# Optimization experiments

Hardware: AMD Instinct MI355X
Metric: run time of the kernel (lower is better)

## Reference

```python
import jax, jax.numpy as jnp
import numpy as np

NPHEN = 64    # number of expert submodels
K = 32        # len(subset1): selected experts / output columns
B = 2048      # batch size
D_IN = 1024   # input feature dim
HID = 2048    # hidden dim of each expert MLP


def setup_inputs() -> dict:
    key = jax.random.key(0)
    k_x, k_s, k_w1, k_b1, k_w2, k_b2 = jax.random.split(key, 6)
    x = jax.random.normal(k_x, (B, D_IN), dtype=jnp.float32)
    subset1 = jax.random.randint(k_s, (K,), 0, NPHEN, dtype=jnp.int64)
    # Expert parameter banks (one 2-layer MLP per phenotype), scaled like torch defaults
    W1 = jax.random.normal(k_w1, (NPHEN, D_IN, HID), dtype=jnp.float32) / np.sqrt(D_IN)
    b1 = jax.random.normal(k_b1, (NPHEN, HID), dtype=jnp.float32) * 0.01
    W2 = jax.random.normal(k_w2, (NPHEN, HID, 1), dtype=jnp.float32) / np.sqrt(HID)
    b2 = jax.random.normal(k_b2, (NPHEN, 1), dtype=jnp.float32) * 0.01
    return {"x": x, "subset1": subset1, "W1": W1, "b1": b1, "W2": W2, "b2": b2}


def reference(x, subset1, W1, b1, W2, b2):
    # Gather the selected experts' weights: [K, D_IN, HID], [K, HID], [K, HID], [K]
    W1s = W1[subset1]
    b1s = b1[subset1]
    W2s = W2[subset1, :, 0]
    b2s = b2[subset1, 0]
    # Batched grouped matmul replacing the per-column Python loop:
    # h[b,k,h] = relu(sum_d x[b,d] * W1s[k,d,h] + b1s[k,h])
    h = jax.nn.relu(jnp.einsum('bd,kdh->bkh', x, W1s) + b1s[None, :, :])
    # predVector[b,k] = sum_h h[b,k,h] * W2s[k,h] + b2s[k]  (== modelList[subset1[k]](x)[:,0])
    pred = jnp.einsum('bkh,kh->bk', h, W2s) + b2s[None, :]
    return pred
```

## Files before the change

kernel.cpp:

```cpp
#include <hip/hip_runtime.h>

#define D_IN 1024
#define HID  2048
#define KSEL 32

typedef __attribute__((ext_vector_type(8))) short short8;
typedef __attribute__((ext_vector_type(4))) float f32x4;

__device__ __forceinline__ short f2bf(float f) {
  union { float f; unsigned u; } c; c.f = f;
  unsigned u = c.u;
  unsigned r = (u + 0x7fffu + ((u >> 16) & 1u)) >> 16;
  return (short)(r & 0xffffu);
}

__global__ __launch_bounds__(256) void conv_x_kernel(const float* __restrict__ x,
                                                     short* __restrict__ Apanel) {
  int tid = blockIdx.x * 256 + threadIdx.x;
  int k8 = tid & 3;
  int m  = (tid >> 2) & 127;
  int ks = (tid >> 9) & 31;
  int mt = tid >> 14;
  const float* src = x + (size_t)(mt * 128 + m) * D_IN + ks * 32 + k8 * 8;
  short8 v;
#pragma unroll
  for (int j = 0; j < 8; ++j) v[j] = f2bf(src[j]);
  *(short8*)(Apanel + (size_t)tid * 8) = v;
}

__global__ __launch_bounds__(256) void conv_w1_kernel(const float* __restrict__ W1,
                                                      const int* __restrict__ subset,
                                                      short* __restrict__ Bpanel) {
  int bid = blockIdx.x;
  int ks = bid & 31;
  int nt = (bid >> 5) & 15;
  int kk = bid >> 9;
  int p  = subset[kk];
  __shared__ float tile[32][129];
  int t = threadIdx.x;
  const float* src = W1 + ((size_t)p * D_IN + ks * 32) * HID + nt * 128;
#pragma unroll
  for (int i = 0; i < 4; ++i) {
    int dl = i * 8 + (t >> 5);
    int hl = (t & 31) * 4;
    float4 v = *(const float4*)(src + (size_t)dl * HID + hl);
    tile[dl][hl] = v.x; tile[dl][hl + 1] = v.y;
    tile[dl][hl + 2] = v.z; tile[dl][hl + 3] = v.w;
  }
  __syncthreads();
  short* dst = Bpanel + (size_t)((kk * 16 + nt) * 32 + ks) * 4096;
#pragma unroll
  for (int j = 0; j < 2; ++j) {
    int n  = j * 64 + (t >> 2);
    int d8 = (t & 3) * 8;
    short8 v;
#pragma unroll
    for (int dd = 0; dd < 8; ++dd) v[dd] = f2bf(tile[d8 + dd][n]);
    *(short8*)(dst + n * 32 + d8) = v;
  }
}

__global__ __launch_bounds__(256) void init_out_kernel(const int* __restrict__ subset,
                                                       const float* __restrict__ b2,
                                                       float* __restrict__ out) {
  int i = blockIdx.x * 256 + threadIdx.x;
  out[i] = b2[subset[i & 31]];
}

__device__ __forceinline__ void load_lds16(const short* g, short* l) {
  __builtin_amdgcn_global_load_lds((const __attribute__((address_space(1))) void*)g,
                                   (__attribute__((address_space(3))) void*)l,
                                   16, 0, 0);
}

__global__ __launch_bounds__(256) void gemm_kernel(const short* __restrict__ Apanel,
                                                   const short* __restrict__ Bpanel,
                                                   const int* __restrict__ subset,
                                                   const float* __restrict__ b1,
                                                   const float* __restrict__ W2,
                                                   float* __restrict__ out) {
  __shared__ __align__(16) short Atile[4096];
  __shared__ __align__(16) short Btile[4096];

  int id = blockIdx.x;
  int xcd = id & 7;
  int chunk = id >> 3;
  int kk = xcd * 4 + (chunk >> 8);
  int nt = (chunk >> 4) & 15;
  int mt = chunk & 15;

  int tid  = threadIdx.x;
  int wave = tid >> 6;
  int lane = tid & 63;
  int wm = wave >> 1, wn = wave & 1;
  int ml = lane & 15;
  int kq = lane >> 4;

  const short* Abase = Apanel + (size_t)mt * (32 * 4096);
  const short* Bbase = Bpanel + (size_t)((kk * 16 + nt)) * (32 * 4096);

  short* AldsBase0 = Atile + (wave * 64) * 8;
  short* AldsBase1 = Atile + (256 + wave * 64) * 8;
  short* BldsBase0 = Btile + (wave * 64) * 8;
  short* BldsBase1 = Btile + (256 + wave * 64) * 8;

  f32x4 acc[4][4] = {};

  const short8* Ar = (const short8*)Atile;
  const short8* Br = (const short8*)Btile;
  int arow = wm * 64 + ml;
  int brow = wn * 64 + ml;

  for (int ks = 0; ks < 32; ++ks) {
    const short* ga = Abase + ks * 4096;
    const short* gb = Bbase + ks * 4096;
    load_lds16(ga + tid * 8,         AldsBase0);
    load_lds16(ga + (256 + tid) * 8, AldsBase1);
    load_lds16(gb + tid * 8,         BldsBase0);
    load_lds16(gb + (256 + tid) * 8, BldsBase1);
    __syncthreads();

    short8 a[4], b[4];
#pragma unroll
    for (int ti = 0; ti < 4; ++ti) a[ti] = Ar[(arow + ti * 16) * 4 + kq];
#pragma unroll
    for (int tj = 0; tj < 4; ++tj) b[tj] = Br[(brow + tj * 16) * 4 + kq];
#pragma unroll
    for (int ti = 0; ti < 4; ++ti)
#pragma unroll
      for (int tj = 0; tj < 4; ++tj)
        acc[ti][tj] = __builtin_amdgcn_mfma_f32_16x16x32_bf16(a[ti], b[tj],
                                                              acc[ti][tj], 0, 0, 0);
    __syncthreads();
  }

  int sk = subset[kk];
  const float* b1p = b1 + (size_t)sk * HID + nt * 128 + wn * 64;
  const float* w2p = W2 + (size_t)sk * HID + nt * 128 + wn * 64;
  float b1v[4], w2v[4];
#pragma unroll
  for (int tj = 0; tj < 4; ++tj) {
    int n = tj * 16 + ml;
    b1v[tj] = b1p[n];
    w2v[tj] = w2p[n];
  }
  float part[4][4];
#pragma unroll
  for (int ti = 0; ti < 4; ++ti)
#pragma unroll
    for (int r = 0; r < 4; ++r) {
      float s = 0.f;
#pragma unroll
      for (int tj = 0; tj < 4; ++tj) {
        float h = acc[ti][tj][r] + b1v[tj];
        h = h > 0.f ? h : 0.f;
        s += h * w2v[tj];
      }
      part[ti][r] = s;
    }
#pragma unroll
  for (int off = 1; off < 16; off <<= 1) {
#pragma unroll
    for (int ti = 0; ti < 4; ++ti)
#pragma unroll
      for (int r = 0; r < 4; ++r)
        part[ti][r] += __shfl_xor(part[ti][r], off, 64);
  }
  if (ml == 0) {
    int mbase = mt * 128 + wm * 64 + kq * 4;
#pragma unroll
    for (int ti = 0; ti < 4; ++ti)
#pragma unroll
      for (int r = 0; r < 4; ++r)
        atomicAdd(out + (size_t)(mbase + ti * 16 + r) * KSEL + kk, part[ti][r]);
  }
}

extern "C" void kernel_launch(void* const* d_in, const int* in_sizes, int n_in,
                              void* d_out, int out_size, void* d_ws, size_t ws_size,
                              hipStream_t stream) {
  const float* x      = (const float*)d_in[0];
  const int*   subset = (const int*)d_in[1];
  const float* W1     = (const float*)d_in[2];
  const float* b1     = (const float*)d_in[3];
  const float* W2     = (const float*)d_in[4];
  const float* b2     = (const float*)d_in[5];
  float* out = (float*)d_out;

  short* Apanel = (short*)d_ws;
  short* Bpanel = (short*)((char*)d_ws + (size_t)4 * 1024 * 1024);

  conv_x_kernel<<<1024, 256, 0, stream>>>(x, Apanel);
  conv_w1_kernel<<<16384, 256, 0, stream>>>(W1, subset, Bpanel);
  init_out_kernel<<<256, 256, 0, stream>>>(subset, b2, out);
  gemm_kernel<<<8192, 256, 0, stream>>>(Apanel, Bpanel, subset, b1, W2, out);
}
```

Before: 1.013 ms.

## Restructure W1 conversion kernel with direct global-to-LDS loads and per-block h-chunk loop

```diff
diff --git a/kernel.cpp b/kernel.cpp
--- a/kernel.cpp
+++ b/kernel.cpp
@@ -12,6 +12,12 @@
   unsigned u = c.u;
   unsigned r = (u + 0x7fffu + ((u >> 16) & 1u)) >> 16;
   return (short)(r & 0xffffu);
+}
+
+__device__ __forceinline__ void load_lds16(const void* g, void* l) {
+  __builtin_amdgcn_global_load_lds((const __attribute__((address_space(1))) void*)g,
+                                   (__attribute__((address_space(3))) void*)l,
+                                   16, 0, 0);
 }
 
 __global__ __launch_bounds__(256) void conv_x_kernel(const float* __restrict__ x,
@@ -33,30 +39,38 @@
                                                       short* __restrict__ Bpanel) {
   int bid = blockIdx.x;
   int ks = bid & 31;
-  int nt = (bid >> 5) & 15;
-  int kk = bid >> 9;
+  int kk = bid >> 5;
   int p  = subset[kk];
-  __shared__ float tile[32][129];
+  __shared__ __align__(16) float tile[32][260];
   int t = threadIdx.x;
-  const float* src = W1 + ((size_t)p * D_IN + ks * 32) * HID + nt * 128;
-#pragma unroll
-  for (int i = 0; i < 4; ++i) {
-    int dl = i * 8 + (t >> 5);
-    int hl = (t & 31) * 4;
-    float4 v = *(const float4*)(src + (size_t)dl * HID + hl);
-    tile[dl][hl] = v.x; tile[dl][hl + 1] = v.y;
-    tile[dl][hl + 2] = v.z; tile[dl][hl + 3] = v.w;
-  }
-  __syncthreads();
-  short* dst = Bpanel + (size_t)((kk * 16 + nt) * 32 + ks) * 4096;
-#pragma unroll
-  for (int j = 0; j < 2; ++j) {
-    int n  = j * 64 + (t >> 2);
-    int d8 = (t & 3) * 8;
-    short8 v;
-#pragma unroll
-    for (int dd = 0; dd < 8; ++dd) v[dd] = f2bf(tile[d8 + dd][n]);
-    *(short8*)(dst + n * 32 + d8) = v;
+  int wave = t >> 6, lane = t & 63;
+  const float* src = W1 + ((size_t)p * D_IN + ks * 32) * HID;
+  short* dstbase = Bpanel + (size_t)(kk * 16) * (32 * 4096) + (size_t)ks * 4096;
+
+  for (int hc = 0; hc < 8; ++hc) {
+#pragma unroll
+    for (int rr = 0; rr < 8; ++rr) {
+      int row = rr * 4 + wave;
+      const float* g = src + (size_t)row * HID + hc * 256 + lane * 4;
+      load_lds16(g, &tile[row][0]);
+    }
+    __syncthreads();
+#pragma unroll
+    for (int j = 0; j < 2; ++j) {
+      int nt = hc * 2 + j;
+      int n  = t >> 1;
+      int kh = (t & 1) * 16;
+      int col = j * 128 + n;
+      short8 v0, v1;
+#pragma unroll
+      for (int dd = 0; dd < 8; ++dd) v0[dd] = f2bf(tile[kh + dd][col]);
+#pragma unroll
+      for (int dd = 0; dd < 8; ++dd) v1[dd] = f2bf(tile[kh + 8 + dd][col]);
+      short* dst = dstbase + (size_t)nt * (32 * 4096) + n * 32 + kh;
+      *(short8*)dst = v0;
+      *(short8*)(dst + 8) = v1;
+    }
+    __syncthreads();
   }
 }
 
@@ -65,12 +79,6 @@
                                                        float* __restrict__ out) {
   int i = blockIdx.x * 256 + threadIdx.x;
   out[i] = b2[subset[i & 31]];
-}
-
-__device__ __forceinline__ void load_lds16(const short* g, short* l) {
-  __builtin_amdgcn_global_load_lds((const __attribute__((address_space(1))) void*)g,
-                                   (__attribute__((address_space(3))) void*)l,
-                                   16, 0, 0);
 }
 
 __global__ __launch_bounds__(256) void gemm_kernel(const short* __restrict__ Apanel,
@@ -191,7 +199,7 @@
   short* Bpanel = (short*)((char*)d_ws + (size_t)4 * 1024 * 1024);
 
   conv_x_kernel<<<1024, 256, 0, stream>>>(x, Apanel);
-  conv_w1_kernel<<<16384, 256, 0, stream>>>(W1, subset, Bpanel);
+  conv_w1_kernel<<<1024, 256, 0, stream>>>(W1, subset, Bpanel);
   init_out_kernel<<<256, 256, 0, stream>>>(subset, b2, out);
   gemm_kernel<<<8192, 256, 0, stream>>>(Apanel, Bpanel, subset, b1, W2, out);
 }
```

Measured after the change: 989.0 us. -2.4%, faster.
